# Kernel tuning notes

Hardware: AMD Instinct MI355X
Metric: run time of the kernel (lower is better)

Reference implementation:

```python
import jax, jax.numpy as jnp
import numpy as np
from jax import lax

SEGMENTS = 64
KERNEL = 5


def setup_inputs() -> dict:
    key = jax.random.key(0)
    k1, k2, k3 = jax.random.split(key, 3)
    B, S, F = 4, 4096, 1024
    A6 = 512 * 6
    inp = jax.random.normal(k1, (B, S, F), dtype=jnp.float32)
    W = jax.random.normal(k2, (A6, F), dtype=jnp.float32) * (1.0 / np.sqrt(F))
    b = jax.random.normal(k3, (A6,), dtype=jnp.float32) * 0.01
    return {"inp": inp, "W": W, "b": b}


def reference(inp, W, b):
    # Fused projection: [B,S,F] @ [F,6A] -> [B,S,6A]
    x = jnp.einsum('bsf,af->bsa', inp, W) + b
    qry, key, val, seg, loc, out = jnp.split(x, 6, axis=2)  # each [B,S,A]
    B, S, A = out.shape

    # Global aggregated attention branch
    agg = qry.mean(axis=1)                              # [B,A]
    scores = jnp.einsum('ba,bsa->bs', agg, key)         # [B,S]
    w = jax.nn.softmax(scores, axis=1)                  # [B,S]
    ctx = jnp.einsum('bs,bsa->ba', w, val)              # [B,A]
    aggregated = ctx[:, None, :] * out                  # [B,S,A]

    # Segment max-pool branch
    nseg = S // SEGMENTS
    seg4 = seg.reshape(B, nseg, SEGMENTS, A)
    seg_max = seg4.max(axis=2, keepdims=True)           # [B,nseg,1,A]
    segment_max_pooled = (seg_max * out.reshape(B, nseg, SEGMENTS, A)).reshape(B, S, A)

    # Local sliding-window max-pool branch (stride 1, pad KERNEL//2, -inf padding)
    pad = KERNEL // 2
    local_max_pooled = lax.reduce_window(
        loc, -jnp.inf, lax.max,
        window_dimensions=(1, KERNEL, 1),
        window_strides=(1, 1, 1),
        padding=((0, 0), (pad, pad), (0, 0)))           # [B,S,A]

    return aggregated + segment_max_pooled + local_max_pooled
```

## Files before the change

kernel.cpp:

```cpp
#include <hip/hip_runtime.h>
#include <hip/hip_bf16.h>
#include <stdint.h>

#define B_    4
#define S_    4096
#define F_    1024
#define A_    512
#define N3_   1536
#define M_    16384

#define BM    256
#define BK    64
#define NT    (F_ / BK)
#define LDP   266

typedef __attribute__((ext_vector_type(8))) __bf16 bf16x8;
typedef __attribute__((ext_vector_type(4))) float  f32x4;

__device__ __forceinline__ float bflo(unsigned int u) {
  union { unsigned int i; float f; } v; v.i = u << 16; return v.f;
}
__device__ __forceinline__ float bfhi(unsigned int u) {
  union { unsigned int i; float f; } v; v.i = u & 0xffff0000u; return v.f;
}
__device__ __forceinline__ float bf1(unsigned short u) {
  union { unsigned int i; float f; } v; v.i = ((unsigned int)u) << 16; return v.f;
}
__device__ __forceinline__ unsigned short bfc(float f) {
  return __builtin_bit_cast(unsigned short, __float2bfloat16(f));
}

__device__ __forceinline__ ushort4 cvt_bf4(float4 v) {
  ushort4 o;
  o.x = bfc(v.x); o.y = bfc(v.y); o.z = bfc(v.z); o.w = bfc(v.w);
  return o;
}

typedef __attribute__((address_space(3))) unsigned int lds_uint;
typedef const __attribute__((address_space(1))) unsigned int glob_uint;
__device__ __forceinline__ void lds_load16(const void* g, void* l) {
  __builtin_amdgcn_global_load_lds((glob_uint*)g, (lds_uint*)l, 16, 0, 0);
}

__global__ __launch_bounds__(256) void convert_mean_kernel(
    const float* __restrict__ inp, const float* __restrict__ W,
    unsigned short* __restrict__ inp_bf, unsigned short* __restrict__ w_bf,
    float* __restrict__ mu) {
  int blk = blockIdx.x;
  int t   = threadIdx.x;
  int r0  = blk * 32;
  int b   = r0 >> 12;
  float acc0 = 0.f, acc1 = 0.f, acc2 = 0.f, acc3 = 0.f;
  for (int r = 0; r < 32; r++) {
    size_t row = (size_t)(r0 + r);
    float4 v = ((const float4*)(inp + row * F_))[t];
    acc0 += v.x; acc1 += v.y; acc2 += v.z; acc3 += v.w;
    ((ushort4*)(inp_bf + row * F_))[t] = cvt_bf4(v);
  }
  atomicAdd(&mu[b * F_ + t * 4 + 0], acc0);
  atomicAdd(&mu[b * F_ + t * 4 + 1], acc1);
  atomicAdd(&mu[b * F_ + t * 4 + 2], acc2);
  atomicAdd(&mu[b * F_ + t * 4 + 3], acc3);

  const float* Wc = W + (size_t)N3_ * F_;
  const int n4 = (N3_ * F_) / 4;
  for (int i = blk * 256 + t; i < n4; i += 512 * 256) {
    ((ushort4*)w_bf)[i] = cvt_bf4(((const float4*)Wc)[i]);
  }
}

__global__ void agg_kernel(const float* __restrict__ mu, const float* __restrict__ W,
                           const float* __restrict__ bias, float* __restrict__ agg) {
  int gw = blockIdx.x * 4 + (threadIdx.x >> 6);
  int lane = threadIdx.x & 63;
  int b = gw >> 9, a = gw & 511;
  const float4* wr = (const float4*)(W + (size_t)a * F_);
  const float4* mr = (const float4*)(mu + b * F_);
  float s = 0.f;
#pragma unroll
  for (int k = 0; k < 4; k++) {
    float4 wv = wr[lane + 64 * k], mv = mr[lane + 64 * k];
    s += wv.x * mv.x + wv.y * mv.y + wv.z * mv.z + wv.w * mv.w;
  }
  for (int off = 32; off; off >>= 1) s += __shfl_down(s, off);
  if (lane == 0) agg[b * A_ + a] = s * (1.f / S_) + bias[a];
}

__global__ void v_kernel(const float* __restrict__ agg, const float* __restrict__ W,
                         const float* __restrict__ bias, float* __restrict__ v,
                         float* __restrict__ cvec) {
  int fc = blockIdx.x;
  int ac = blockIdx.y;
  int t = threadIdx.x;
  int f = fc * 256 + t;
  const float* Wk = W + (size_t)A_ * F_;
  float s0 = 0.f, s1 = 0.f, s2 = 0.f, s3 = 0.f;
  int a0 = ac * 64;
  for (int a = a0; a < a0 + 64; a++) {
    float wv = Wk[(size_t)a * F_ + f];
    s0 += agg[a] * wv;
    s1 += agg[A_ + a] * wv;
    s2 += agg[2 * A_ + a] * wv;
    s3 += agg[3 * A_ + a] * wv;
  }
  atomicAdd(&v[f], s0);
  atomicAdd(&v[F_ + f], s1);
  atomicAdd(&v[2 * F_ + f], s2);
  atomicAdd(&v[3 * F_ + f], s3);

  if (fc == 0 && ac == 0) {
    int bb = t >> 6, l = t & 63;
    float c = 0.f;
#pragma unroll
    for (int i = 0; i < 8; i++) c += agg[bb * A_ + l + 64 * i] * bias[A_ + l + 64 * i];
    for (int off = 32; off; off >>= 1) c += __shfl_down(c, off);
    if (l == 0) cvec[bb] = c;
  }
}

__global__ void scores_kernel(const unsigned short* __restrict__ inp_bf,
                              const float* __restrict__ v,
                              const float* __restrict__ cvec, float* __restrict__ scores) {
  int lane = threadIdx.x & 63;
  int row = blockIdx.x * 4 + (threadIdx.x >> 6);
  int b = row >> 12;
  const uint4* ip = (const uint4*)(inp_bf + (size_t)row * F_);
  const float4* vp = (const float4*)(v + b * F_);
  float s = 0.f;
#pragma unroll
  for (int k = 0; k < 2; k++) {
    uint4 x = ip[lane + 64 * k];
    float4 va = vp[(lane + 64 * k) * 2];
    float4 vb = vp[(lane + 64 * k) * 2 + 1];
    s += bflo(x.x) * va.x + bfhi(x.x) * va.y + bflo(x.y) * va.z + bfhi(x.y) * va.w +
         bflo(x.z) * vb.x + bfhi(x.z) * vb.y + bflo(x.w) * vb.z + bfhi(x.w) * vb.w;
  }
  for (int off = 32; off; off >>= 1) s += __shfl_down(s, off);
  if (lane == 0) scores[row] = s + cvec[b];
}

__global__ void softmax_kernel(float* __restrict__ sc) {
  __shared__ float red[256];
  int b = blockIdx.x, t = threadIdx.x;
  float* p = sc + b * S_;
  float vals[16];
  float m = -1e30f;
#pragma unroll
  for (int i = 0; i < 16; i++) { vals[i] = p[t + i * 256]; m = fmaxf(m, vals[i]); }
  red[t] = m; __syncthreads();
  for (int o = 128; o; o >>= 1) { if (t < o) red[t] = fmaxf(red[t], red[t + o]); __syncthreads(); }
  m = red[0]; __syncthreads();
  float sum = 0.f;
#pragma unroll
  for (int i = 0; i < 16; i++) { vals[i] = __expf(vals[i] - m); sum += vals[i]; }
  red[t] = sum; __syncthreads();
  for (int o = 128; o; o >>= 1) { if (t < o) red[t] += red[t + o]; __syncthreads(); }
  float inv = 1.f / red[0];
#pragma unroll
  for (int i = 0; i < 16; i++) p[t + i * 256] = vals[i] * inv;
}

__global__ void u_kernel(const unsigned short* __restrict__ inp_bf,
                         const float* __restrict__ w, float* __restrict__ u) {
  int b = blockIdx.z, fc = blockIdx.y, sc = blockIdx.x;
  int t = threadIdx.x;
  int f2 = fc * 512 + t * 2;
  int s0 = sc * 128;
  const float* wp = w + b * S_ + s0;
  const unsigned short* ip = inp_bf + ((size_t)(b * S_ + s0)) * F_ + f2;
  float a0 = 0.f, a1 = 0.f;
  for (int s = 0; s < 128; s++) {
    unsigned int xv = *(const unsigned int*)&ip[(size_t)s * F_];
    float ws = wp[s];
    a0 += ws * bflo(xv);
    a1 += ws * bfhi(xv);
  }
  atomicAdd(&u[b * F_ + f2], a0);
  atomicAdd(&u[b * F_ + f2 + 1], a1);
}

__global__ void ctx_kernel(const float* __restrict__ u, const float* __restrict__ W,
                           const float* __restrict__ bias, float* __restrict__ ctx) {
  int gw = blockIdx.x * 4 + (threadIdx.x >> 6);
  int lane = threadIdx.x & 63;
  int b = gw >> 9, a = gw & 511;
  const float4* wr = (const float4*)(W + (size_t)(2 * A_ + a) * F_);
  const float4* ur = (const float4*)(u + b * F_);
  float s = 0.f;
#pragma unroll
  for (int k = 0; k < 4; k++) {
    float4 wv = wr[lane + 64 * k], uv = ur[lane + 64 * k];
    s += wv.x * uv.x + wv.y * uv.y + wv.z * uv.z + wv.w * uv.w;
  }
  for (int off = 32; off; off >>= 1) s += __shfl_down(s, off);
  if (lane == 0) ctx[b * A_ + a] = s + bias[2 * A_ + a];
}

__global__ __launch_bounds__(512, 2) void gemm_fused(
    const __hip_bfloat16* __restrict__ Abf,
    const __hip_bfloat16* __restrict__ Wbf,
    const float* __restrict__ biasP,
    const float* __restrict__ ctx,
    float* __restrict__ out,
    unsigned short* __restrict__ sideLoc,
    float* __restrict__ sideGO) {
  extern __shared__ unsigned short smem[];
  unsigned short* ldsA = smem;
  unsigned short* ldsB = smem + 32768;
  unsigned short* Xt   = smem;
  float* segred = (float*)((char*)smem + 192 * LDP * 2);

  int bid = blockIdx.x;
  int swz = (bid & 7) * 64 + (bid >> 3);
  int mb = swz >> 3;
  int nb = swz & 7;

  int tid  = threadIdx.x;
  int lane = tid & 63;
  int wv   = tid >> 6;
  int wm   = wv >> 1;
  int wn   = wv & 1;
  int lo   = lane & 15, hi = lane >> 4, sw = lane & 7;

  int bir0 = (((hi * 16)      ^ (sw << 4)) >> 1);
  int bir1 = (((64 + hi * 16) ^ (sw << 4)) >> 1);

  const __hip_bfloat16* Ab = Abf + (size_t)mb * BM * F_;

  int srow = tid >> 3;
  int sel  = ((tid & 7) ^ (srow & 7)) * 8;
  int ldst = wv * 512;

  f32x4 acc[4][6];
#pragma unroll
  for (int i = 0; i < 4; i++)
#pragma unroll
    for (int j = 0; j < 6; j++) acc[i][j] = (f32x4){0.f, 0.f, 0.f, 0.f};

  int aBase = (wm * 64 + lo) * 64;
  int bBase = (wn * 96 + lo) * 64;

#define STG_A(kt_, buf_, r_)                                                              \
  lds_load16(Ab + (size_t)((r_) * 64 + srow) * F_ + (kt_) * BK + sel,                     \
             ldsA + (buf_) * 16384 + (r_) * 4096 + ldst)
#define STG_B(kt_, buf_, q_)                                                              \
  lds_load16(Wbf + (size_t)((q_) * 512 + nb * 64 + srow) * F_ + (kt_) * BK + sel,         \
             ldsB + (buf_) * 12288 + (q_) * 4096 + ldst)

  STG_A(0, 0, 0); STG_A(0, 0, 1); STG_A(0, 0, 2); STG_A(0, 0, 3);
  STG_B(0, 0, 0); STG_B(0, 0, 1); STG_B(0, 0, 2);

  for (int kt = 0; kt < NT; ++kt) {
    int c = kt & 1, nx = c ^ 1;
    bool pf = (kt + 1 < NT);
    const unsigned short* la = ldsA + c * 16384;
    const unsigned short* lb = ldsB + c * 12288;
    bf16x8 af[4][2], bfr[2][2];

    if (pf) {
      STG_A(kt + 1, nx, 0); STG_A(kt + 1, nx, 1); STG_A(kt + 1, nx, 2);
      asm volatile("s_waitcnt vmcnt(3)" ::: "memory");
    } else {
      asm volatile("s_waitcnt vmcnt(0)" ::: "memory");
    }
    __builtin_amdgcn_s_barrier();
#pragma unroll
    for (int i = 0; i < 4; i++) {
      af[i][0] = *(const bf16x8*)&la[aBase + i * 1024 + bir0];
      af[i][1] = *(const bf16x8*)&la[aBase + i * 1024 + bir1];
    }
#pragma unroll
    for (int j = 0; j < 2; j++) {
      bfr[j][0] = *(const bf16x8*)&lb[bBase + j * 1024 + bir0];
      bfr[j][1] = *(const bf16x8*)&lb[bBase + j * 1024 + bir1];
    }
    asm volatile("s_waitcnt lgkmcnt(0)" ::: "memory");
    __builtin_amdgcn_sched_barrier(0);
    __builtin_amdgcn_s_setprio(1);
#pragma unroll
    for (int i = 0; i < 4; i++)
#pragma unroll
      for (int j = 0; j < 2; j++) {
        acc[i][j] = __builtin_amdgcn_mfma_f32_16x16x32_bf16(af[i][0], bfr[j][0], acc[i][j], 0, 0, 0);
        acc[i][j] = __builtin_amdgcn_mfma_f32_16x16x32_bf16(af[i][1], bfr[j][1], acc[i][j], 0, 0, 0);
      }
    __builtin_amdgcn_s_setprio(0);
    __builtin_amdgcn_s_barrier();

#pragma unroll
    for (int j = 0; j < 2; j++) {
      bfr[j][0] = *(const bf16x8*)&lb[bBase + (2 + j) * 1024 + bir0];
      bfr[j][1] = *(const bf16x8*)&lb[bBase + (2 + j) * 1024 + bir1];
    }
    if (pf) { STG_A(kt + 1, nx, 3); STG_B(kt + 1, nx, 0); }
    __builtin_amdgcn_s_barrier();
    asm volatile("s_waitcnt lgkmcnt(0)" ::: "memory");
    __builtin_amdgcn_sched_barrier(0);
    __builtin_amdgcn_s_setprio(1);
#pragma unroll
    for (int i = 0; i < 4; i++)
#pragma unroll
      for (int j = 0; j < 2; j++) {
        acc[i][2 + j] = __builtin_amdgcn_mfma_f32_16x16x32_bf16(af[i][0], bfr[j][0], acc[i][2 + j], 0, 0, 0);
        acc[i][2 + j] = __builtin_amdgcn_mfma_f32_16x16x32_bf16(af[i][1], bfr[j][1], acc[i][2 + j], 0, 0, 0);
      }
    __builtin_amdgcn_s_setprio(0);
    __builtin_amdgcn_s_barrier();

#pragma unroll
    for (int j = 0; j < 2; j++) {
      bfr[j][0] = *(const bf16x8*)&lb[bBase + (4 + j) * 1024 + bir0];
      bfr[j][1] = *(const bf16x8*)&lb[bBase + (4 + j) * 1024 + bir1];
    }
    if (pf) { STG_B(kt + 1, nx, 1); STG_B(kt + 1, nx, 2); }
    __builtin_amdgcn_s_barrier();
    asm volatile("s_waitcnt lgkmcnt(0)" ::: "memory");
    __builtin_amdgcn_sched_barrier(0);
    __builtin_amdgcn_s_setprio(1);
#pragma unroll
    for (int i = 0; i < 4; i++)
#pragma unroll
      for (int j = 0; j < 2; j++) {
        acc[i][4 + j] = __builtin_amdgcn_mfma_f32_16x16x32_bf16(af[i][0], bfr[j][0], acc[i][4 + j], 0, 0, 0);
        acc[i][4 + j] = __builtin_amdgcn_mfma_f32_16x16x32_bf16(af[i][1], bfr[j][1], acc[i][4 + j], 0, 0, 0);
      }
    __builtin_amdgcn_s_setprio(0);
    __builtin_amdgcn_s_barrier();
  }
#undef STG_A
#undef STG_B

  float bias_r[6];
#pragma unroll
  for (int fj = 0; fj < 6; fj++) {
    int cl = wn * 96 + fj * 16 + lo;
    bias_r[fj] = biasP[(cl >> 6) * 512 + nb * 64 + (cl & 63)];
  }
#pragma unroll
  for (int fi = 0; fi < 4; fi++) {
#pragma unroll
    for (int fj = 0; fj < 6; fj++) {
      int cl = wn * 96 + fj * 16 + lo;
      int r  = wm * 64 + fi * 16 + hi * 4;
      float v0 = acc[fi][fj][0] + bias_r[fj];
      float v1 = acc[fi][fj][1] + bias_r[fj];
      float v2 = acc[fi][fj][2] + bias_r[fj];
      float v3 = acc[fi][fj][3] + bias_r[fj];
      unsigned int u01 = (unsigned int)bfc(v0) | ((unsigned int)bfc(v1) << 16);
      unsigned int u23 = (unsigned int)bfc(v2) | ((unsigned int)bfc(v3) << 16);
      *(unsigned int*)&Xt[cl * LDP + r]     = u01;
      *(unsigned int*)&Xt[cl * LDP + r + 2] = u23;
    }
  }
  __syncthreads();

  if (tid < 256) {
    int seg = tid >> 6, c = tid & 63;
    int base = c * LDP + seg * 64;
    float m = -1e30f;
#pragma unroll
    for (int k = 0; k < 32; k++) {
      unsigned int u = *(const unsigned int*)&Xt[base + 2 * k];
      m = fmaxf(m, fmaxf(bflo(u), bfhi(u)));
    }
    segred[seg * 64 + c] = m;
  }
  __syncthreads();

  {
    int c  = lane;
    int r0 = wv * 32;
    int b  = mb >> 4;
    int gcol = nb * 64 + c;
    float g = ctx[b * 512 + gcol] + segred[(r0 >> 6) * 64 + c];
    int lbase = (64 + c) * LDP;
    int obase = (128 + c) * LDP;
    float lw0 = bf1(Xt[lbase + max(r0 - 2, 0)]);
    float lw1 = bf1(Xt[lbase + max(r0 - 1, 0)]);
    float lw2 = bf1(Xt[lbase + r0]);
    float lw3 = bf1(Xt[lbase + r0 + 1]);
    size_t obase_g = ((size_t)(mb * 256 + r0)) * 512 + gcol;
#pragma unroll
    for (int j = 0; j < 32; j++) {
      int rn = min(r0 + j + 2, 255);
      float lw4 = bf1(Xt[lbase + rn]);
      float lm = fmaxf(fmaxf(fmaxf(lw0, lw1), fmaxf(lw2, lw3)), lw4);
      float o = bf1(Xt[obase + r0 + j]);
      out[obase_g + (size_t)j * 512] = g * o + lm;
      lw0 = lw1; lw1 = lw2; lw2 = lw3; lw3 = lw4;
    }
  }

  if (tid < 256) {
    int rsel = tid >> 6, c = tid & 63;
    int r = (rsel < 2) ? rsel : (252 + rsel);
    int b = mb >> 4;
    float g = ctx[b * 512 + nb * 64 + c] + segred[(r >> 6) * 64 + c];
    float o = bf1(Xt[(128 + c) * LDP + r]);
    int gr = mb * 4 + rsel;
    sideLoc[gr * 512 + nb * 64 + c] = Xt[(64 + c) * LDP + r];
    sideGO[gr * 512 + nb * 64 + c]  = g * o;
  }
}

__global__ void fixup_kernel(const unsigned short* __restrict__ sideLoc,
                             const float* __restrict__ sideGO,
                             float* __restrict__ out) {
  int rb = blockIdx.x;
  int tb = rb & 15;
  int t = threadIdx.x;
  int rsel = t >> 6, cq = t & 63;
#pragma unroll
  for (int k = 0; k < 8; k++) {
    int c = cq * 8 + k;
    float miss;
    int rl;
    if (rsel == 0) {
      if (tb == 0) continue;
      miss = fmaxf(bf1(sideLoc[((rb - 1) * 4 + 2) * 512 + c]),
                   bf1(sideLoc[((rb - 1) * 4 + 3) * 512 + c]));
      rl = 0;
    } else if (rsel == 1) {
      if (tb == 0) continue;
      miss = bf1(sideLoc[((rb - 1) * 4 + 3) * 512 + c]);
      rl = 1;
    } else if (rsel == 2) {
      if (tb == 15) continue;
      miss = bf1(sideLoc[((rb + 1) * 4 + 0) * 512 + c]);
      rl = 254;
    } else {
      if (tb == 15) continue;
      miss = fmaxf(bf1(sideLoc[((rb + 1) * 4 + 0) * 512 + c]),
                   bf1(sideLoc[((rb + 1) * 4 + 1) * 512 + c]));
      rl = 255;
    }
    size_t oi = ((size_t)rb * 256 + rl) * 512 + c;
    float cand = sideGO[(rb * 4 + rsel) * 512 + c] + miss;
    out[oi] = fmaxf(out[oi], cand);
  }
}

extern "C" void kernel_launch(void* const* d_in, const int* in_sizes, int n_in,
                              void* d_out, int out_size, void* d_ws, size_t ws_size,
                              hipStream_t stream) {
  const float* inp  = (const float*)d_in[0];
  const float* W    = (const float*)d_in[1];
  const float* bias = (const float*)d_in[2];
  float* out = (float*)d_out;
  char* ws = (char*)d_ws;

  const size_t INP_OFF  = 0;
  const size_t W_OFF    = 33554432;
  const size_t MU_OFF   = 36700160;
  const size_t U_OFF    = MU_OFF + 16384;
  const size_t V_OFF    = U_OFF + 16384;
  const size_t CV_OFF   = V_OFF + 16384;
  const size_t AGG_OFF  = CV_OFF + 256;
  const size_t CTX_OFF  = AGG_OFF + 8192;
  const size_t SC_OFF   = CTX_OFF + 8192;
  const size_t SL_OFF   = SC_OFF + 65536;
  const size_t SG_OFF   = SL_OFF + 262144;

  unsigned short* inp_bf = (unsigned short*)(ws + INP_OFF);
  unsigned short* w_bf   = (unsigned short*)(ws + W_OFF);
  float* mu     = (float*)(ws + MU_OFF);
  float* u      = (float*)(ws + U_OFF);
  float* v      = (float*)(ws + V_OFF);
  float* cvec   = (float*)(ws + CV_OFF);
  float* agg    = (float*)(ws + AGG_OFF);
  float* ctx    = (float*)(ws + CTX_OFF);
  float* scores = (float*)(ws + SC_OFF);
  unsigned short* sideLoc = (unsigned short*)(ws + SL_OFF);
  float* sideGO = (float*)(ws + SG_OFF);

  hipFuncSetAttribute(reinterpret_cast<const void*>(gemm_fused),
                      hipFuncAttributeMaxDynamicSharedMemorySize, 114688);

  hipMemsetAsync(ws + MU_OFF, 0, 3 * 16384 + 256, stream);
  convert_mean_kernel<<<512, 256, 0, stream>>>(inp, W, inp_bf, w_bf, mu);
  agg_kernel<<<512, 256, 0, stream>>>(mu, W, bias, agg);
  v_kernel<<<dim3(4, 8), 256, 0, stream>>>(agg, W, bias, v, cvec);
  scores_kernel<<<4096, 256, 0, stream>>>(inp_bf, v, cvec, scores);
  softmax_kernel<<<4, 256, 0, stream>>>(scores);
  u_kernel<<<dim3(32, 2, 4), 256, 0, stream>>>(inp_bf, scores, u);
  ctx_kernel<<<512, 256, 0, stream>>>(u, W, bias, ctx);
  gemm_fused<<<512, 512, 114688, stream>>>((const __hip_bfloat16*)inp_bf,
                                           (const __hip_bfloat16*)w_bf,
                                           bias + 3 * A_, ctx, out, sideLoc, sideGO);
  fixup_kernel<<<64, 256, 0, stream>>>(sideLoc, sideGO, out);
}
```

Measured before the change: 128.1 us.

## Software-pipeline LDS fragment loads across MFMA phases and next k-tile

```diff
diff --git a/kernel.cpp b/kernel.cpp
--- a/kernel.cpp
+++ b/kernel.cpp
@@ -16,6 +16,8 @@
 
 typedef __attribute__((ext_vector_type(8))) __bf16 bf16x8;
 typedef __attribute__((ext_vector_type(4))) float  f32x4;
+
+#define MFMA(a, b, c) __builtin_amdgcn_mfma_f32_16x16x32_bf16((a), (b), (c), 0, 0, 0)
 
 __device__ __forceinline__ float bflo(unsigned int u) {
   union { unsigned int i; float f; } v; v.i = u << 16; return v.f;
@@ -247,33 +249,31 @@
   lds_load16(Wbf + (size_t)((q_) * 512 + nb * 64 + srow) * F_ + (kt_) * BK + sel,         \
              ldsB + (buf_) * 12288 + (q_) * 4096 + ldst)
 
+  bf16x8 af[4][2], b01[2][2], b23[2][2], b45[2][2];
+
   STG_A(0, 0, 0); STG_A(0, 0, 1); STG_A(0, 0, 2); STG_A(0, 0, 3);
   STG_B(0, 0, 0); STG_B(0, 0, 1); STG_B(0, 0, 2);
+  asm volatile("s_waitcnt vmcnt(0)" ::: "memory");
+  __builtin_amdgcn_s_barrier();
+#pragma unroll
+  for (int i = 0; i < 4; i++) {
+    af[i][0] = *(const bf16x8*)&ldsA[aBase + i * 1024 + bir0];
+    af[i][1] = *(const bf16x8*)&ldsA[aBase + i * 1024 + bir1];
+  }
+#pragma unroll
+  for (int j = 0; j < 2; j++) {
+    b01[j][0] = *(const bf16x8*)&ldsB[bBase + j * 1024 + bir0];
+    b01[j][1] = *(const bf16x8*)&ldsB[bBase + j * 1024 + bir1];
+  }
 
   for (int kt = 0; kt < NT; ++kt) {
     int c = kt & 1, nx = c ^ 1;
     bool pf = (kt + 1 < NT);
-    const unsigned short* la = ldsA + c * 16384;
-    const unsigned short* lb = ldsB + c * 12288;
-    bf16x8 af[4][2], bfr[2][2];
-
-    if (pf) {
-      STG_A(kt + 1, nx, 0); STG_A(kt + 1, nx, 1); STG_A(kt + 1, nx, 2);
-      asm volatile("s_waitcnt vmcnt(3)" ::: "memory");
-    } else {
-      asm volatile("s_waitcnt vmcnt(0)" ::: "memory");
-    }
-    __builtin_amdgcn_s_barrier();
-#pragma unroll
-    for (int i = 0; i < 4; i++) {
-      af[i][0] = *(const bf16x8*)&la[aBase + i * 1024 + bir0];
-      af[i][1] = *(const bf16x8*)&la[aBase + i * 1024 + bir1];
-    }
-#pragma unroll
-    for (int j = 0; j < 2; j++) {
-      bfr[j][0] = *(const bf16x8*)&lb[bBase + j * 1024 + bir0];
-      bfr[j][1] = *(const bf16x8*)&lb[bBase + j * 1024 + bir1];
-    }
+    const unsigned short* lb  = ldsB + c * 12288;
+    const unsigned short* lan = ldsA + nx * 16384;
+    const unsigned short* lbn = ldsB + nx * 12288;
+
+    if (pf) { STG_A(kt + 1, nx, 0); STG_A(kt + 1, nx, 1); STG_A(kt + 1, nx, 2); STG_A(kt + 1, nx, 3); }
     asm volatile("s_waitcnt lgkmcnt(0)" ::: "memory");
     __builtin_amdgcn_sched_barrier(0);
     __builtin_amdgcn_s_setprio(1);
@@ -281,19 +281,18 @@
     for (int i = 0; i < 4; i++)
 #pragma unroll
       for (int j = 0; j < 2; j++) {
-        acc[i][j] = __builtin_amdgcn_mfma_f32_16x16x32_bf16(af[i][0], bfr[j][0], acc[i][j], 0, 0, 0);
-        acc[i][j] = __builtin_amdgcn_mfma_f32_16x16x32_bf16(af[i][1], bfr[j][1], acc[i][j], 0, 0, 0);
+        acc[i][j] = MFMA(af[i][0], b01[j][0], acc[i][j]);
+        acc[i][j] = MFMA(af[i][1], b01[j][1], acc[i][j]);
       }
     __builtin_amdgcn_s_setprio(0);
+#pragma unroll
+    for (int j = 0; j < 2; j++) {
+      b23[j][0] = *(const bf16x8*)&lb[bBase + (2 + j) * 1024 + bir0];
+      b23[j][1] = *(const bf16x8*)&lb[bBase + (2 + j) * 1024 + bir1];
+    }
     __builtin_amdgcn_s_barrier();
 
-#pragma unroll
-    for (int j = 0; j < 2; j++) {
-      bfr[j][0] = *(const bf16x8*)&lb[bBase + (2 + j) * 1024 + bir0];
-      bfr[j][1] = *(const bf16x8*)&lb[bBase + (2 + j) * 1024 + bir1];
-    }
-    if (pf) { STG_A(kt + 1, nx, 3); STG_B(kt + 1, nx, 0); }
-    __builtin_amdgcn_s_barrier();
+    if (pf) { STG_B(kt + 1, nx, 0); STG_B(kt + 1, nx, 1); STG_B(kt + 1, nx, 2); }
     asm volatile("s_waitcnt lgkmcnt(0)" ::: "memory");
     __builtin_amdgcn_sched_barrier(0);
     __builtin_amdgcn_s_setprio(1);
@@ -301,19 +300,17 @@
     for (int i = 0; i < 4; i++)
 #pragma unroll
       for (int j = 0; j < 2; j++) {
-        acc[i][2 + j] = __builtin_amdgcn_mfma_f32_16x16x32_bf16(af[i][0], bfr[j][0], acc[i][2 + j], 0, 0, 0);
-        acc[i][2 + j] = __builtin_amdgcn_mfma_f32_16x16x32_bf16(af[i][1], bfr[j][1], acc[i][2 + j], 0, 0, 0);
+        acc[i][2 + j] = MFMA(af[i][0], b23[j][0], acc[i][2 + j]);
+        acc[i][2 + j] = MFMA(af[i][1], b23[j][1], acc[i][2 + j]);
       }
     __builtin_amdgcn_s_setprio(0);
+#pragma unroll
+    for (int j = 0; j < 2; j++) {
+      b45[j][0] = *(const bf16x8*)&lb[bBase + (4 + j) * 1024 + bir0];
+      b45[j][1] = *(const bf16x8*)&lb[bBase + (4 + j) * 1024 + bir1];
+    }
     __builtin_amdgcn_s_barrier();
 
-#pragma unroll
-    for (int j = 0; j < 2; j++) {
-      bfr[j][0] = *(const bf16x8*)&lb[bBase + (4 + j) * 1024 + bir0];
-      bfr[j][1] = *(const bf16x8*)&lb[bBase + (4 + j) * 1024 + bir1];
-    }
-    if (pf) { STG_B(kt + 1, nx, 1); STG_B(kt + 1, nx, 2); }
-    __builtin_amdgcn_s_barrier();
     asm volatile("s_waitcnt lgkmcnt(0)" ::: "memory");
     __builtin_amdgcn_sched_barrier(0);
     __builtin_amdgcn_s_setprio(1);
@@ -321,11 +318,24 @@
     for (int i = 0; i < 4; i++)
 #pragma unroll
       for (int j = 0; j < 2; j++) {
-        acc[i][4 + j] = __builtin_amdgcn_mfma_f32_16x16x32_bf16(af[i][0], bfr[j][0], acc[i][4 + j], 0, 0, 0);
-        acc[i][4 + j] = __builtin_amdgcn_mfma_f32_16x16x32_bf16(af[i][1], bfr[j][1], acc[i][4 + j], 0, 0, 0);
+        acc[i][4 + j] = MFMA(af[i][0], b45[j][0], acc[i][4 + j]);
+        acc[i][4 + j] = MFMA(af[i][1], b45[j][1], acc[i][4 + j]);
       }
     __builtin_amdgcn_s_setprio(0);
+    if (pf) asm volatile("s_waitcnt vmcnt(0)" ::: "memory");
     __builtin_amdgcn_s_barrier();
+    if (pf) {
+#pragma unroll
+      for (int i = 0; i < 4; i++) {
+        af[i][0] = *(const bf16x8*)&lan[aBase + i * 1024 + bir0];
+        af[i][1] = *(const bf16x8*)&lan[aBase + i * 1024 + bir1];
+      }
+#pragma unroll
+      for (int j = 0; j < 2; j++) {
+        b01[j][0] = *(const bf16x8*)&lbn[bBase + j * 1024 + bir0];
+        b01[j][1] = *(const bf16x8*)&lbn[bBase + j * 1024 + bir1];
+      }
+    }
   }
 #undef STG_A
 #undef STG_B
```

After: 126.8 us. No clear change (-1.0%).
